# Performance work log

Hardware: AMD Instinct MI355X
Metric: run time of the kernel (lower is better)

Reference implementation:

```python
import jax, jax.numpy as jnp
import numpy as np

B, S, D = 8, 1024, 128
EPS = 1e-7
LN_EPS = 1e-3  # keras LayerNormalization default


def setup_inputs() -> dict:
    key = jax.random.key(0)
    ks = jax.random.split(key, 8)
    sd = 1.0 / np.sqrt(D)
    return {
        "x": jax.random.normal(ks[0], (B, S, D), jnp.float32),
        "Wq": jax.random.normal(ks[1], (D, D), jnp.float32) * sd,
        "bq": jnp.zeros((D,), jnp.float32),
        "Wm": jax.random.normal(ks[2], (D, D), jnp.float32) * sd,
        "bm": jnp.zeros((D,), jnp.float32),
        "Ww": jax.random.normal(ks[3], (D, 1), jnp.float32) * sd,
        "bw": jnp.zeros((1,), jnp.float32),
        "Wc": jax.random.normal(ks[4], (D, 1), jnp.float32) * sd,
        "bc": jnp.zeros((1,), jnp.float32),
        "emb_map": jax.random.normal(ks[5], (D, D, D), jnp.float32) * 0.02,
        "gamma": jnp.ones((D,), jnp.float32),
        "beta": jnp.zeros((D,), jnp.float32),
    }


def reference(x, Wq, bq, Wm, bm, Ww, bw, Wc, bc, emb_map, gamma, beta):
    b_, s_, d_ = x.shape
    q = x @ Wq + bq                      # [B,S,D]
    m = jax.nn.sigmoid(x @ Wm + bm)      # [B,S,D]
    w = jax.nn.relu(x @ Ww + bw)         # [B,S,1]
    c = jax.nn.relu(x @ Wc + bc)         # [B,S,1]

    # distances: for query pos i, preceding pos j (j<i) has distance i-j
    idx = jnp.arange(s_)
    dist = (idx[:, None] - idx[None, :]).astype(x.dtype)   # [S,S]
    valid = dist > 0                                       # strict causal
    # cosh positional decay, zero outside causal window -> [B,S,S]
    pe = jnp.where(valid[None], 1.0 / jnp.cosh((dist[None] - c) / (w + EPS)), 0.0)

    # angle between (pe * x_j * m_i + eps) and (q_i + eps), expanded analytically
    qp = q + EPS
    t1 = jnp.einsum('bjd,bid->bij', x, m * qp)             # sum_d x_j m_i q'_i
    s1 = jnp.einsum('bjd,bid->bij', x, m)                  # sum_d x_j m_i
    s2 = jnp.einsum('bjd,bid->bij', x * x, m * m)          # sum_d (x_j m_i)^2
    dot = pe * t1 + EPS * jnp.sum(qp, axis=-1)[:, :, None]
    na = jnp.sqrt(pe * pe * s2 + 2.0 * EPS * pe * s1 + d_ * EPS * EPS)
    nb = jnp.linalg.norm(qp, axis=-1)[:, :, None]
    cos = jnp.where(valid[None], dot / (na * nb), 0.0)
    angle = jnp.where(valid[None], jnp.arccos(cos), 0.0)   # [B,S,S]

    # query_result_i = sum_j pe*angle * x_j  -> [B,S,D]
    qr = jnp.einsum('bij,bjd->bid', pe * angle, x)

    # embedding matrix: current_token (rows) outer query_result (cols),
    # contracted against rank-3 map: out[b,s,d] = sum_{j,k} x[b,s,j] qr[b,s,k] map[d,j,k]
    em = jnp.einsum('bsj,bsk->bsjk', x, qr).reshape(b_, s_, d_ * d_)
    mapped = em @ emb_map.reshape(d_, d_ * d_).T           # [B,S,D]

    res = mapped + x
    mu = jnp.mean(res, axis=-1, keepdims=True)
    var = jnp.var(res, axis=-1, keepdims=True)
    out = (res - mu) / jnp.sqrt(var + LN_EPS) * gamma + beta
    return out  # dropout is identity at inference
```

## Files before the change

### kernel.cpp

```cpp
#include <hip/hip_runtime.h>
#include <hip/hip_bf16.h>
#include <math.h>

#define DD 128
#define SS 1024
#define NROWS 8192
#define EPSF 1e-7f
#define LN_EPSF 1e-3f
#define TCUT 30.0f

typedef __attribute__((ext_vector_type(8))) short bf16x8;
typedef __attribute__((ext_vector_type(4))) float f32x4;
typedef __attribute__((ext_vector_type(16))) float f32x16;

__device__ __forceinline__ void gload_lds16(const void* g, void* l) {
    __builtin_amdgcn_global_load_lds(
        (const __attribute__((address_space(1))) unsigned int*)g,
        (__attribute__((address_space(3))) unsigned int*)l, 16, 0, 0);
}
__device__ __forceinline__ short f2bf(float v) {
    union { __hip_bfloat16 h; short s; } u;
    u.h = __float2bfloat16(v);
    return u.s;
}
__device__ __forceinline__ float bf2f(short s) {
    union { __hip_bfloat16 h; short s; } u; u.s = s;
    return __bfloat162float(u.h);
}
__device__ __forceinline__ unsigned int pack_bf16(float lo, float hi) {
    unsigned int r;
    asm("v_cvt_pk_bf16_f32 %0, %1, %2" : "=v"(r) : "v"(lo), "v"(hi));
    return r;
}
__device__ __forceinline__ float u2f(unsigned int u) {
    union { unsigned int u; float f; } c; c.u = u; return c.f;
}

__global__ __launch_bounds__(256) void k0a_emb(const float* __restrict__ emb,
                                               short* __restrict__ embB) {
    __shared__ float lt[128][132];
    int j = blockIdx.x, t = threadIdx.x;
    {
        int d = t >> 1, kh = (t & 1) * 64;
        const float* src = emb + (size_t)d * 16384 + (size_t)j * 128 + kh;
#pragma unroll
        for (int q = 0; q < 16; ++q)
            *(float4*)&lt[d][kh + q * 4] = *(const float4*)(src + q * 4);
    }
    __syncthreads();
#pragma unroll
    for (int i = 0; i < 8; ++i) {
        int idx = i * 256 + t;
        int l = idx & 63, s = (idx >> 6) & 7, dt = (idx >> 9) & 3;
        const float* p = &lt[dt * 32 + (l & 31)][s * 16 + (l >> 5) * 8];
        union { bf16x8 v; short sa[8]; } ob;
#pragma unroll
        for (int e = 0; e < 8; ++e) ob.sa[e] = f2bf(p[e]);
        *(bf16x8*)(embB + (size_t)j * 16384 + dt * 4096 + s * 512 + (size_t)l * 8) = ob.v;
    }
}

__global__ __launch_bounds__(256) void k0w_split(const float* __restrict__ Wq,
        const float* __restrict__ Wm, short* __restrict__ Wfrag) {
    int T = blockIdx.x * 256 + threadIdx.x;
    int e = T & 7, l = (T >> 3) & 63, ks = (T >> 9) & 3, nt = (T >> 11) & 7,
        mat = (T >> 14) & 1;
    int k = ks * 32 + ((l >> 4) & 3) * 8 + e;
    int c = nt * 16 + (l & 15);
    float v = (mat ? Wm : Wq)[k * 128 + c];
    short h = f2bf(v);
    float lo = v - bf2f(h);
    Wfrag[((((size_t)(mat * 2 + 0) * 8 + nt) * 4 + ks) * 64 + l) * 8 + e] = h;
    Wfrag[((((size_t)(mat * 2 + 1) * 8 + nt) * 4 + ks) * 64 + l) * 8 + e] = f2bf(lo);
}

__global__ __launch_bounds__(256) void k0c_xsplit(const float* __restrict__ x,
        const float* __restrict__ Ww, const float* __restrict__ bw,
        const float* __restrict__ Wc, const float* __restrict__ bc,
        short* __restrict__ xh2, short* __restrict__ xl2,
        float* __restrict__ scal) {
    __shared__ float xs[32][129];
    int rb = blockIdx.x, t = threadIdx.x;
    {
        int r = t >> 3, d0 = (t & 7) * 16;
        const float4* src = (const float4*)(x + (size_t)(rb * 32 + r) * 128 + d0);
#pragma unroll
        for (int q = 0; q < 4; ++q) *(float4*)&xs[r][d0 + q * 4] = src[q];
    }
    __syncthreads();
    int ks = (t >> 5) & 3, rf = t >> 7, l0 = (t & 31) * 2;
    union { bf16x8 v[2]; short s[16]; } hb, lb;
#pragma unroll
    for (int li = 0; li < 2; ++li) {
        int l = l0 + li;
        const float* p = &xs[rf * 16 + (l & 15)][ks * 32 + ((l >> 4) & 3) * 8];
#pragma unroll
        for (int e = 0; e < 8; ++e) {
            float v = p[e];
            short h = f2bf(v);
            hb.s[li * 8 + e] = h;
            lb.s[li * 8 + e] = f2bf(v - bf2f(h));
        }
    }
    {
        short* d1 = xh2 + (size_t)rb * 4096 + (size_t)t * 16;
        short* d2 = xl2 + (size_t)rb * 4096 + (size_t)t * 16;
        *(bf16x8*)d1 = hb.v[0]; *(bf16x8*)(d1 + 8) = hb.v[1];
        *(bf16x8*)d2 = lb.v[0]; *(bf16x8*)(d2 + 8) = lb.v[1];
    }
    int rr = t >> 3, seg = t & 7;
    float pw = 0.f, pc = 0.f;
#pragma unroll
    for (int dq = 0; dq < 16; ++dq) {
        float xv = xs[rr][seg * 16 + dq];
        pw = fmaf(xv, Ww[seg * 16 + dq], pw);
        pc = fmaf(xv, Wc[seg * 16 + dq], pc);
    }
    pw += __shfl_xor(pw, 1); pw += __shfl_xor(pw, 2); pw += __shfl_xor(pw, 4);
    pc += __shfl_xor(pc, 1); pc += __shfl_xor(pc, 2); pc += __shfl_xor(pc, 4);
    if (seg == 0) {
        scal[(size_t)(rb * 32 + rr) * 4 + 0] = fmaxf(pw + bw[0], 0.f);
        scal[(size_t)(rb * 32 + rr) * 4 + 1] = fmaxf(pc + bc[0], 0.f);
    }
}

__global__ __launch_bounds__(256) void k1_mfma(
    const short* __restrict__ xh2, const short* __restrict__ xl2,
    const short* __restrict__ Wfrag,
    const float* __restrict__ bq, const float* __restrict__ bm,
    float* __restrict__ mq, float* __restrict__ mo, float* __restrict__ scal)
{
    __shared__ __align__(16) short wl[65536];
    __shared__ float red[32][4][2];
    int t = threadIdx.x, w = t >> 6, l = t & 63;
    int l15 = l & 15, g = l >> 4;
    int row0 = blockIdx.x * 32;
#pragma unroll
    for (int it = 0; it < 32; ++it)
        gload_lds16(Wfrag + (size_t)(it * 256 + t) * 8, wl + (size_t)(it * 256 + w * 64) * 8);
    const short* xb  = xh2 + (size_t)blockIdx.x * 4096;
    const short* xlb = xl2 + (size_t)blockIdx.x * 4096;
    bf16x8 Ah[2][4], Al[2][4];
#pragma unroll
    for (int rf = 0; rf < 2; ++rf)
#pragma unroll
        for (int ks = 0; ks < 4; ++ks) {
            size_t o = ((size_t)(rf * 4 + ks) * 64 + l) * 8;
            Ah[rf][ks] = *(const bf16x8*)(xb + o);
            Al[rf][ks] = *(const bf16x8*)(xlb + o);
        }
    __syncthreads();
    f32x4 accq[2][2] = {}, accm[2][2] = {};
#pragma unroll
    for (int ntp = 0; ntp < 2; ++ntp) {
        int nt = w * 2 + ntp;
#pragma unroll
        for (int ks = 0; ks < 4; ++ks) {
            bf16x8 bhq = *(const bf16x8*)(wl + ((size_t)(0  + nt) * 4 + ks) * 512 + l * 8);
            bf16x8 blq = *(const bf16x8*)(wl + ((size_t)(8  + nt) * 4 + ks) * 512 + l * 8);
            bf16x8 bhm = *(const bf16x8*)(wl + ((size_t)(16 + nt) * 4 + ks) * 512 + l * 8);
            bf16x8 blm = *(const bf16x8*)(wl + ((size_t)(24 + nt) * 4 + ks) * 512 + l * 8);
#pragma unroll
            for (int rf = 0; rf < 2; ++rf) {
                accq[rf][ntp] = __builtin_amdgcn_mfma_f32_16x16x32_bf16(Ah[rf][ks], bhq, accq[rf][ntp], 0, 0, 0);
                accq[rf][ntp] = __builtin_amdgcn_mfma_f32_16x16x32_bf16(Ah[rf][ks], blq, accq[rf][ntp], 0, 0, 0);
                accq[rf][ntp] = __builtin_amdgcn_mfma_f32_16x16x32_bf16(Al[rf][ks], bhq, accq[rf][ntp], 0, 0, 0);
                accm[rf][ntp] = __builtin_amdgcn_mfma_f32_16x16x32_bf16(Ah[rf][ks], bhm, accm[rf][ntp], 0, 0, 0);
                accm[rf][ntp] = __builtin_amdgcn_mfma_f32_16x16x32_bf16(Ah[rf][ks], blm, accm[rf][ntp], 0, 0, 0);
                accm[rf][ntp] = __builtin_amdgcn_mfma_f32_16x16x32_bf16(Al[rf][ks], bhm, accm[rf][ntp], 0, 0, 0);
            }
        }
    }
    float sq1[2][4] = {{0,0,0,0},{0,0,0,0}};
    float sq2[2][4] = {{0,0,0,0},{0,0,0,0}};
#pragma unroll
    for (int ntp = 0; ntp < 2; ++ntp) {
        int c = (w * 2 + ntp) * 16 + l15;
        float bqv = bq[c] + EPSF, bmv = bm[c];
#pragma unroll
        for (int rf = 0; rf < 2; ++rf)
#pragma unroll
            for (int reg = 0; reg < 4; ++reg) {
                int rloc = rf * 16 + g * 4 + reg;
                float qp = accq[rf][ntp][reg] + bqv;
                float mv = 1.0f / (1.0f + expf(-(accm[rf][ntp][reg] + bmv)));
                size_t o = (size_t)(row0 + rloc) * 128 + c;
                mq[o] = mv * qp;
                mo[o] = mv;
                sq1[rf][reg] += qp;
                sq2[rf][reg] += qp * qp;
            }
    }
#pragma unroll
    for (int rf = 0; rf < 2; ++rf)
#pragma unroll
        for (int reg = 0; reg < 4; ++reg) {
            float a = sq1[rf][reg], b = sq2[rf][reg];
            a += __shfl_xor(a, 1); a += __shfl_xor(a, 2);
            a += __shfl_xor(a, 4); a += __shfl_xor(a, 8);
            b += __shfl_xor(b, 1); b += __shfl_xor(b, 2);
            b += __shfl_xor(b, 4); b += __shfl_xor(b, 8);
            if (l15 == 0) {
                red[rf * 16 + g * 4 + reg][w][0] = a;
                red[rf * 16 + g * 4 + reg][w][1] = b;
            }
        }
    __syncthreads();
    if (t < 32) {
        float a = red[t][0][0] + red[t][1][0] + red[t][2][0] + red[t][3][0];
        float b = red[t][0][1] + red[t][1][1] + red[t][2][1] + red[t][3][1];
        scal[(size_t)(row0 + t) * 4 + 2] = a;
        scal[(size_t)(row0 + t) * 4 + 3] = sqrtf(b);
    }
}

__global__ __launch_bounds__(256) void k2_qr(
    const float* __restrict__ x,
    const float* __restrict__ mq, const float* __restrict__ mo,
    const float* __restrict__ scal, short* __restrict__ qrh2)
{
    int row = blockIdx.x;
    int i = row & (SS - 1);
    const float* xb = x + (size_t)(row - i) * DD;
    int t = threadIdx.x, w = t >> 6, l = t & 63;
    int sub = l >> 4, q = l & 15;
    int qo = q * 8;

    float mqv[8], mov[8];
    {
        const float* mp = mq + (size_t)row * DD + qo;
        float4 a = *(const float4*)mp, b = *(const float4*)(mp + 4);
        mqv[0] = a.x; mqv[1] = a.y; mqv[2] = a.z; mqv[3] = a.w;
        mqv[4] = b.x; mqv[5] = b.y; mqv[6] = b.z; mqv[7] = b.w;
        const float* op = mo + (size_t)row * DD + qo;
        float4 c = *(const float4*)op, d = *(const float4*)(op + 4);
        mov[0] = c.x; mov[1] = c.y; mov[2] = c.z; mov[3] = c.w;
        mov[4] = d.x; mov[5] = d.y; mov[6] = d.z; mov[7] = d.w;
    }
    float wv = scal[row * 4 + 0], cv = scal[row * 4 + 1];
    float sumqp = scal[row * 4 + 2], nb = scal[row * 4 + 3];
    float wi = wv + EPSF;
    float dmaxf = cv + TCUT * wi;
    int dmax = (dmaxf >= (float)i) ? i : (int)dmaxf;

    float acc[8] = {0.f, 0.f, 0.f, 0.f, 0.f, 0.f, 0.f, 0.f};
    int nit = (dmax + 15) >> 4;
    int dbase = 1 + w * 4 + sub;
    for (int it = 0; it < nit; ++it) {
        int dist = dbase + it * 16;
        float xv[8];
        if (dist <= dmax) {
            const float* xp = xb + (size_t)(i - dist) * DD + qo;
            float4 a = *(const float4*)xp, b = *(const float4*)(xp + 4);
            xv[0] = a.x; xv[1] = a.y; xv[2] = a.z; xv[3] = a.w;
            xv[4] = b.x; xv[5] = b.y; xv[6] = b.z; xv[7] = b.w;
        } else {
#pragma unroll
            for (int e = 0; e < 8; ++e) xv[e] = 0.f;
        }
        float t1 = 0.f, s1 = 0.f, s2 = 0.f;
#pragma unroll
        for (int e = 0; e < 8; ++e) {
            float xm = xv[e] * mov[e];
            t1 = fmaf(xv[e], mqv[e], t1);
            s1 += xm;
            s2 = fmaf(xm, xm, s2);
        }
#pragma unroll
        for (int off = 1; off < 16; off <<= 1) {
            t1 += __shfl_xor(t1, off);
            s1 += __shfl_xor(s1, off);
            s2 += __shfl_xor(s2, off);
        }
        float tt = ((float)dist - cv) / wi;
        float pe = 1.0f / coshf(tt);
        float dotv = fmaf(pe, t1, EPSF * sumqp);
        float na = sqrtf(fmaf(pe * pe, s2,
                         fmaf(2.0f * EPSF * pe, s1, (float)DD * EPSF * EPSF)));
        float cosv = fminf(1.0f, fmaxf(-1.0f, dotv / (na * nb)));
        float ang = acosf(cosv);
        float wgt = pe * ang;
#pragma unroll
        for (int e = 0; e < 8; ++e) acc[e] = fmaf(wgt, xv[e], acc[e]);
    }
#pragma unroll
    for (int e = 0; e < 8; ++e) {
        acc[e] += __shfl_xor(acc[e], 16);
        acc[e] += __shfl_xor(acc[e], 32);
    }
    __shared__ float sq[4][DD];
    if (l < 16) {
#pragma unroll
        for (int e = 0; e < 8; ++e) sq[w][qo + e] = acc[e];
    }
    __syncthreads();
    if (t < DD) {
        float v = sq[0][t] + sq[1][t] + sq[2][t] + sq[3][t];
        int rbq = row >> 7, rr = row & 127, rt2 = rr >> 5, lp = rr & 31;
        int k = t;
        qrh2[(((size_t)(rbq * 4 + rt2) * 8 + (k >> 4)) * 64
              + (lp + 32 * ((k >> 3) & 1))) * 8 + (k & 7)] = f2bf(v);
    }
}

__global__ __launch_bounds__(256, 2) void k3_gemm(
    const float* __restrict__ x, const short* __restrict__ embB,
    const short* __restrict__ qrh2, float* __restrict__ part)
{
    __shared__ float xt[32][68];
    __shared__ float sof[64][128];
    int t = threadIdx.x, w = t >> 6, l = t & 63;
    int l31 = l & 31, hi = l >> 5;
    int dh = w & 1, sh = w >> 1;
    int rb = blockIdx.x, js = blockIdx.y;

    {
        int r = t >> 2, q = t & 3;
        const float* xp = x + (size_t)(rb * 64 + r) * 128 + js * 32 + q * 8;
        float4 a = *(const float4*)xp, b = *(const float4*)(xp + 4);
        xt[q * 8 + 0][r] = a.x; xt[q * 8 + 1][r] = a.y;
        xt[q * 8 + 2][r] = a.z; xt[q * 8 + 3][r] = a.w;
        xt[q * 8 + 4][r] = b.x; xt[q * 8 + 5][r] = b.y;
        xt[q * 8 + 6][r] = b.z; xt[q * 8 + 7][r] = b.w;
    }

    unsigned int qrp[2][4][4];
#pragma unroll
    for (int rt = 0; rt < 2; ++rt) {
        int R32 = rb * 2 + rt;
#pragma unroll
        for (int s = 0; s < 4; ++s) {
            union { bf16x8 v; unsigned int u[4]; } qb;
            qb.v = *(const bf16x8*)(qrh2
                + (((size_t)R32 * 8 + sh * 4 + s) * 64 + l) * 8);
#pragma unroll
            for (int p = 0; p < 4; ++p) qrp[rt][s][p] = qb.u[p];
        }
    }

    const short* Bbase = embB + (size_t)(js * 32) * 16384
                         + (size_t)(dh * 2) * 4096 + (size_t)(sh * 4) * 512
                         + (size_t)l * 8;

    f32x16 acc[2][2];
#pragma unroll
    for (int rt = 0; rt < 2; ++rt)
#pragma unroll
        for (int i = 0; i < 2; ++i)
#pragma unroll
            for (int q = 0; q < 16; ++q) acc[rt][i][q] = 0.f;

#define LOADB(BN, JJ)                                                       \
    {                                                                       \
        const short* bp_ = Bbase + (size_t)(JJ) * 16384;                    \
        _Pragma("unroll")                                                   \
        for (int i = 0; i < 2; ++i)                                         \
            _Pragma("unroll")                                               \
            for (int s = 0; s < 4; ++s)                                     \
                BN[i][s] = *(const bf16x8*)(bp_ + i * 4096 + s * 512);      \
    }

#define COMPUTE(BN, JJ)                                                     \
    {                                                                       \
        float xs0 = xt[JJ][l31], xs1 = xt[JJ][32 + l31];                    \
        _Pragma("unroll")                                                   \
        for (int s = 0; s < 4; ++s) {                                       \
            union { bf16x8 v; unsigned int u[4]; } a0, a1;                  \
            _Pragma("unroll")                                               \
            for (int p = 0; p < 4; ++p) {                                   \
                unsigned int q0 = qrp[0][s][p], q1 = qrp[1][s][p];          \
                a0.u[p] = pack_bf16(u2f(q0 << 16) * xs0,                    \
                                    u2f(q0 & 0xFFFF0000u) * xs0);           \
                a1.u[p] = pack_bf16(u2f(q1 << 16) * xs1,                    \
                                    u2f(q1 & 0xFFFF0000u) * xs1);           \
            }                                                               \
            acc[0][0] = __builtin_amdgcn_mfma_f32_32x32x16_bf16(            \
                a0.v, BN[0][s], acc[0][0], 0, 0, 0);                        \
            acc[0][1] = __builtin_amdgcn_mfma_f32_32x32x16_bf16(            \
                a0.v, BN[1][s], acc[0][1], 0, 0, 0);                        \
            acc[1][0] = __builtin_amdgcn_mfma_f32_32x32x16_bf16(            \
                a1.v, BN[0][s], acc[1][0], 0, 0, 0);                        \
            acc[1][1] = __builtin_amdgcn_mfma_f32_32x32x16_bf16(            \
                a1.v, BN[1][s], acc[1][1], 0, 0, 0);                        \
        }                                                                   \
    }

    bf16x8 B0[2][4], B1[2][4];
    LOADB(B0, 0)
    __syncthreads();

#pragma unroll 1
    for (int jj = 0; jj < 32; jj += 2) {
        if (jj + 1 < 32) LOADB(B1, jj + 1)
        COMPUTE(B0, jj)
        if (jj + 2 < 32) LOADB(B0, jj + 2)
        COMPUTE(B1, jj + 1)
    }
#undef LOADB
#undef COMPUTE

    __syncthreads();
    if (sh == 0) {
#pragma unroll
        for (int rt = 0; rt < 2; ++rt)
#pragma unroll
            for (int i = 0; i < 2; ++i)
#pragma unroll
                for (int q = 0; q < 16; ++q) {
                    int r = rt * 32 + (q & 3) + 8 * (q >> 2) + 4 * hi;
                    sof[r][(dh * 2 + i) * 32 + l31] = acc[rt][i][q];
                }
    }
    __syncthreads();
    if (sh == 1) {
#pragma unroll
        for (int rt = 0; rt < 2; ++rt)
#pragma unroll
            for (int i = 0; i < 2; ++i)
#pragma unroll
                for (int q = 0; q < 16; ++q) {
                    int r = rt * 32 + (q & 3) + 8 * (q >> 2) + 4 * hi;
                    sof[r][(dh * 2 + i) * 32 + l31] += acc[rt][i][q];
                }
    }
    __syncthreads();
#pragma unroll
    for (int i = 0; i < 8; ++i) {
        int idx = i * 256 + t;
        int r = idx >> 5, c4 = (idx & 31) * 4;
        float4 v = *(const float4*)&sof[r][c4];
        *(float4*)(part + (size_t)js * (NROWS * DD)
                   + (size_t)(rb * 64 + r) * 128 + c4) = v;
    }
}

__global__ __launch_bounds__(256) void k4_ln(
    const float* __restrict__ x, const float* __restrict__ part,
    const float* __restrict__ gamma, const float* __restrict__ beta,
    float* __restrict__ out)
{
    int wave = threadIdx.x >> 6, lane = threadIdx.x & 63;
    int row = blockIdx.x * 4 + wave;
    size_t base = (size_t)row * DD;
    float r0 = x[base + lane], r1 = x[base + lane + 64];
#pragma unroll
    for (int p = 0; p < 4; ++p) {
        r0 += part[(size_t)p * NROWS * DD + base + lane];
        r1 += part[(size_t)p * NROWS * DD + base + lane + 64];
    }
    float s = r0 + r1, s2 = r0 * r0 + r1 * r1;
#pragma unroll
    for (int off = 32; off > 0; off >>= 1) {
        s += __shfl_xor(s, off);
        s2 += __shfl_xor(s2, off);
    }
    float mu = s * (1.0f / DD);
    float var = s2 * (1.0f / DD) - mu * mu;
    var = fmaxf(var, 0.0f);
    float rs = rsqrtf(var + LN_EPSF);
    out[base + lane] = (r0 - mu) * rs * gamma[lane] + beta[lane];
    out[base + lane + 64] = (r1 - mu) * rs * gamma[lane + 64] + beta[lane + 64];
}

extern "C" void kernel_launch(void* const* d_in, const int* in_sizes, int n_in,
                              void* d_out, int out_size, void* d_ws, size_t ws_size,
                              hipStream_t stream) {
    const float* x     = (const float*)d_in[0];
    const float* Wq    = (const float*)d_in[1];
    const float* bq    = (const float*)d_in[2];
    const float* Wm    = (const float*)d_in[3];
    const float* bm    = (const float*)d_in[4];
    const float* Ww    = (const float*)d_in[5];
    const float* bw    = (const float*)d_in[6];
    const float* Wc    = (const float*)d_in[7];
    const float* bc    = (const float*)d_in[8];
    const float* emb   = (const float*)d_in[9];
    const float* gamma = (const float*)d_in[10];
    const float* beta  = (const float*)d_in[11];
    float* out = (float*)d_out;
    float* ws  = (float*)d_ws;

    short* embB  = (short*)ws;
    short* qrh2  = (short*)(ws + 1048576);
    float* scal  = ws + 1572864;
    float* part  = ws + 1605632;
    float* tr    = ws + 1605632;
    short* xh2   = (short*)tr;
    short* xl2   = (short*)(tr + 524288);
    float* mq    = tr + 1048576;
    float* mo    = tr + 2097152;
    short* Wfrag = (short*)(tr + 3145728);

    hipLaunchKernelGGL(k0a_emb,   dim3(128),    dim3(256), 0, stream, emb, embB);
    hipLaunchKernelGGL(k0w_split, dim3(256),    dim3(256), 0, stream, Wq, Wm, Wfrag);
    hipLaunchKernelGGL(k0c_xsplit,dim3(256),    dim3(256), 0, stream,
                       x, Ww, bw, Wc, bc, xh2, xl2, scal);
    hipLaunchKernelGGL(k1_mfma,   dim3(256),    dim3(256), 0, stream,
                       xh2, xl2, Wfrag, bq, bm, mq, mo, scal);
    hipLaunchKernelGGL(k2_qr,     dim3(8192),   dim3(256), 0, stream,
                       x, mq, mo, scal, qrh2);
    hipLaunchKernelGGL(k3_gemm,   dim3(128, 4), dim3(256), 0, stream,
                       x, embB, qrh2, part);
    hipLaunchKernelGGL(k4_ln,     dim3(2048),   dim3(256), 0, stream,
                       x, part, gamma, beta, out);
}
```

Measured before the change: 89.52 us.

## Split k3 GEMM over output-column halves and write bf16 partials without LDS reduction

The k3 grid gains a dimension that splits the 128 output columns into two halves, halving per-block accumulators and B fragments so four blocks can fit per CU. The LDS reduction of the two K-half waves is removed: each wave writes its own bf16 partial directly to global memory, and k4_ln now sums eight bf16 partial slices instead of four fp32 ones. A-fragment construction is hoisted ahead of the MFMA sequence, which is wrapped in s_setprio. Storing partials in bf16 adds rounding error, and the scattered 2-byte stores may coalesce poorly. The qr fragments are also reloaded by twice as many blocks.

```diff
diff --git a/kernel.cpp b/kernel.cpp
--- a/kernel.cpp
+++ b/kernel.cpp
@@ -303,16 +303,15 @@
     }
 }
 
-__global__ __launch_bounds__(256, 2) void k3_gemm(
+__global__ __launch_bounds__(256, 4) void k3_gemm(
     const float* __restrict__ x, const short* __restrict__ embB,
-    const short* __restrict__ qrh2, float* __restrict__ part)
+    const short* __restrict__ qrh2, short* __restrict__ partb)
 {
-    __shared__ float xt[32][68];
-    __shared__ float sof[64][128];
+    __shared__ float xt[32][66];
     int t = threadIdx.x, w = t >> 6, l = t & 63;
     int l31 = l & 31, hi = l >> 5;
     int dh = w & 1, sh = w >> 1;
-    int rb = blockIdx.x, js = blockIdx.y;
+    int rb = blockIdx.x, dq = blockIdx.y, js = blockIdx.z;
 
     {
         int r = t >> 2, q = t & 3;
@@ -339,53 +338,49 @@
     }
 
     const short* Bbase = embB + (size_t)(js * 32) * 16384
-                         + (size_t)(dh * 2) * 4096 + (size_t)(sh * 4) * 512
+                         + (size_t)(dq * 2 + dh) * 4096 + (size_t)(sh * 4) * 512
                          + (size_t)l * 8;
 
-    f32x16 acc[2][2];
+    f32x16 acc[2];
 #pragma unroll
     for (int rt = 0; rt < 2; ++rt)
 #pragma unroll
-        for (int i = 0; i < 2; ++i)
-#pragma unroll
-            for (int q = 0; q < 16; ++q) acc[rt][i][q] = 0.f;
+        for (int q = 0; q < 16; ++q) acc[rt][q] = 0.f;
 
 #define LOADB(BN, JJ)                                                       \
     {                                                                       \
         const short* bp_ = Bbase + (size_t)(JJ) * 16384;                    \
         _Pragma("unroll")                                                   \
-        for (int i = 0; i < 2; ++i)                                         \
-            _Pragma("unroll")                                               \
-            for (int s = 0; s < 4; ++s)                                     \
-                BN[i][s] = *(const bf16x8*)(bp_ + i * 4096 + s * 512);      \
+        for (int s = 0; s < 4; ++s)                                         \
+            BN[s] = *(const bf16x8*)(bp_ + s * 512);                        \
     }
 
 #define COMPUTE(BN, JJ)                                                     \
     {                                                                       \
         float xs0 = xt[JJ][l31], xs1 = xt[JJ][32 + l31];                    \
+        union { bf16x8 v; unsigned int u[4]; } af[2][4];                    \
         _Pragma("unroll")                                                   \
-        for (int s = 0; s < 4; ++s) {                                       \
-            union { bf16x8 v; unsigned int u[4]; } a0, a1;                  \
+        for (int s = 0; s < 4; ++s)                                         \
             _Pragma("unroll")                                               \
             for (int p = 0; p < 4; ++p) {                                   \
                 unsigned int q0 = qrp[0][s][p], q1 = qrp[1][s][p];          \
-                a0.u[p] = pack_bf16(u2f(q0 << 16) * xs0,                    \
-                                    u2f(q0 & 0xFFFF0000u) * xs0);           \
-                a1.u[p] = pack_bf16(u2f(q1 << 16) * xs1,                    \
-                                    u2f(q1 & 0xFFFF0000u) * xs1);           \
+                af[0][s].u[p] = pack_bf16(u2f(q0 << 16) * xs0,              \
+                                          u2f(q0 & 0xFFFF0000u) * xs0);     \
+                af[1][s].u[p] = pack_bf16(u2f(q1 << 16) * xs1,              \
+                                          u2f(q1 & 0xFFFF0000u) * xs1);     \
             }                                                               \
-            acc[0][0] = __builtin_amdgcn_mfma_f32_32x32x16_bf16(            \
-                a0.v, BN[0][s], acc[0][0], 0, 0, 0);                        \
-            acc[0][1] = __builtin_amdgcn_mfma_f32_32x32x16_bf16(            \
-                a0.v, BN[1][s], acc[0][1], 0, 0, 0);                        \
-            acc[1][0] = __builtin_amdgcn_mfma_f32_32x32x16_bf16(            \
-                a1.v, BN[0][s], acc[1][0], 0, 0, 0);                        \
-            acc[1][1] = __builtin_amdgcn_mfma_f32_32x32x16_bf16(            \
-                a1.v, BN[1][s], acc[1][1], 0, 0, 0);                        \
+        __builtin_amdgcn_s_setprio(1);                                      \
+        _Pragma("unroll")                                                   \
+        for (int s = 0; s < 4; ++s) {                                       \
+            acc[0] = __builtin_amdgcn_mfma_f32_32x32x16_bf16(               \
+                af[0][s].v, BN[s], acc[0], 0, 0, 0);                        \
+            acc[1] = __builtin_amdgcn_mfma_f32_32x32x16_bf16(               \
+                af[1][s].v, BN[s], acc[1], 0, 0, 0);                        \
         }                                                                   \
-    }
-
-    bf16x8 B0[2][4], B1[2][4];
+        __builtin_amdgcn_s_setprio(0);                                      \
+    }
+
+    bf16x8 B0[4], B1[4];
     LOADB(B0, 0)
     __syncthreads();
 
@@ -399,43 +394,20 @@
 #undef LOADB
 #undef COMPUTE
 
-    __syncthreads();
-    if (sh == 0) {
-#pragma unroll
-        for (int rt = 0; rt < 2; ++rt)
-#pragma unroll
-            for (int i = 0; i < 2; ++i)
-#pragma unroll
-                for (int q = 0; q < 16; ++q) {
-                    int r = rt * 32 + (q & 3) + 8 * (q >> 2) + 4 * hi;
-                    sof[r][(dh * 2 + i) * 32 + l31] = acc[rt][i][q];
-                }
-    }
-    __syncthreads();
-    if (sh == 1) {
-#pragma unroll
-        for (int rt = 0; rt < 2; ++rt)
-#pragma unroll
-            for (int i = 0; i < 2; ++i)
-#pragma unroll
-                for (int q = 0; q < 16; ++q) {
-                    int r = rt * 32 + (q & 3) + 8 * (q >> 2) + 4 * hi;
-                    sof[r][(dh * 2 + i) * 32 + l31] += acc[rt][i][q];
-                }
-    }
-    __syncthreads();
-#pragma unroll
-    for (int i = 0; i < 8; ++i) {
-        int idx = i * 256 + t;
-        int r = idx >> 5, c4 = (idx & 31) * 4;
-        float4 v = *(const float4*)&sof[r][c4];
-        *(float4*)(part + (size_t)js * (NROWS * DD)
-                   + (size_t)(rb * 64 + r) * 128 + c4) = v;
+    size_t pbase = (size_t)(js * 2 + sh) * ((size_t)NROWS * DD);
+    int dcol = dq * 64 + dh * 32 + l31;
+#pragma unroll
+    for (int rt = 0; rt < 2; ++rt) {
+#pragma unroll
+        for (int q = 0; q < 16; ++q) {
+            int rowg = rb * 64 + rt * 32 + (q & 3) + 8 * (q >> 2) + 4 * hi;
+            partb[pbase + (size_t)rowg * 128 + dcol] = f2bf(acc[rt][q]);
+        }
     }
 }
 
 __global__ __launch_bounds__(256) void k4_ln(
-    const float* __restrict__ x, const float* __restrict__ part,
+    const float* __restrict__ x, const short* __restrict__ partb,
     const float* __restrict__ gamma, const float* __restrict__ beta,
     float* __restrict__ out)
 {
@@ -444,9 +416,9 @@
     size_t base = (size_t)row * DD;
     float r0 = x[base + lane], r1 = x[base + lane + 64];
 #pragma unroll
-    for (int p = 0; p < 4; ++p) {
-        r0 += part[(size_t)p * NROWS * DD + base + lane];
-        r1 += part[(size_t)p * NROWS * DD + base + lane + 64];
+    for (int p = 0; p < 8; ++p) {
+        r0 += bf2f(partb[(size_t)p * 1048576 + base + lane]);
+        r1 += bf2f(partb[(size_t)p * 1048576 + base + lane + 64]);
     }
     float s = r0 + r1, s2 = r0 * r0 + r1 * r1;
 #pragma unroll
@@ -483,7 +455,7 @@
     short* embB  = (short*)ws;
     short* qrh2  = (short*)(ws + 1048576);
     float* scal  = ws + 1572864;
-    float* part  = ws + 1605632;
+    short* partb = (short*)(ws + 1605632);
     float* tr    = ws + 1605632;
     short* xh2   = (short*)tr;
     short* xl2   = (short*)(tr + 524288);
@@ -499,8 +471,8 @@
                        xh2, xl2, Wfrag, bq, bm, mq, mo, scal);
     hipLaunchKernelGGL(k2_qr,     dim3(8192),   dim3(256), 0, stream,
                        x, mq, mo, scal, qrh2);
-    hipLaunchKernelGGL(k3_gemm,   dim3(128, 4), dim3(256), 0, stream,
-                       x, embB, qrh2, part);
+    hipLaunchKernelGGL(k3_gemm,   dim3(128, 2, 4), dim3(256), 0, stream,
+                       x, embB, qrh2, partb);
     hipLaunchKernelGGL(k4_ln,     dim3(2048),   dim3(256), 0, stream,
-                       x, part, gamma, beta, out);
-}
+                       x, partb, gamma, beta, out);
+}
```

Measured after the change: 324.8 us. +262.8%, slower.
